# Performance work log

Measured on AMD Instinct MI355X. Metric: run time of the kernel, lower is better.

The kernel has to match this reference:

```python
import jax, jax.numpy as jnp
import numpy as np

HIDDEN = 1280
NUM_HEADS = 16
HEAD_DIM = HIDDEN // NUM_HEADS  # 80
T = 2048
NEG_INF = -1e9


def apply_rope(x, rope):
    # x: [B, T, N, H], rope: [T, H//2]
    half = x.shape[-1] // 2
    xr, xi = x[..., :half], x[..., half:]
    cos = jnp.cos(rope)[None, :, None, :]
    sin = jnp.sin(rope)[None, :, None, :]
    return jnp.concatenate([xr * cos - xi * sin, xr * sin + xi * cos], axis=-1)


def setup_inputs() -> dict:
    key = jax.random.key(0)
    ks = jax.random.split(key, 7)
    x = jax.random.normal(ks[0], (T, 1, HIDDEN), dtype=jnp.float32)
    rotary_pos_emb = jax.random.normal(ks[1], (T, HEAD_DIM // 2), dtype=jnp.float32)
    segment_ids = jnp.sort(jax.random.randint(ks[2], (T,), 0, 8, dtype=jnp.int32))
    s = 0.02
    qkv_kernel = jax.random.normal(ks[3], (HIDDEN, 3 * HIDDEN), dtype=jnp.float32) * s
    qkv_bias = jax.random.normal(ks[4], (3 * HIDDEN,), dtype=jnp.float32) * s
    proj_kernel = jax.random.normal(ks[5], (HIDDEN, HIDDEN), dtype=jnp.float32) * s
    proj_bias = jax.random.normal(ks[6], (HIDDEN,), dtype=jnp.float32) * s
    return {"x": x, "rotary_pos_emb": rotary_pos_emb, "segment_ids": segment_ids,
            "qkv_kernel": qkv_kernel, "qkv_bias": qkv_bias,
            "proj_kernel": proj_kernel, "proj_bias": proj_bias}


def reference(x, rotary_pos_emb, segment_ids, qkv_kernel, qkv_bias, proj_kernel, proj_bias):
    Tt, B, D = x.shape  # B == 1
    N, H = NUM_HEADS, HEAD_DIM
    qkv = x @ qkv_kernel + qkv_bias                      # [T, B, 3D]
    q, k, v = jnp.split(qkv, 3, axis=-1)
    # [T, B, N, H] -> [B, T, N, H]
    q = jnp.transpose(q.reshape(Tt, B, N, H), (1, 0, 2, 3))
    k = jnp.transpose(k.reshape(Tt, B, N, H), (1, 0, 2, 3))
    v = jnp.transpose(v.reshape(Tt, B, N, H), (1, 0, 2, 3))
    q = apply_rope(q, rotary_pos_emb)
    k = apply_rope(k, rotary_pos_emb)
    # segment-masked attention (non-causal), sm_scale = 1/sqrt(H)
    scale = 1.0 / np.sqrt(H).astype(np.float32)
    scores = jnp.einsum('bqnh,bknh->bnqk', q, k) * scale  # [B, N, T, T]
    mask = segment_ids[:, None] == segment_ids[None, :]   # [T, T]
    scores = jnp.where(mask[None, None], scores, NEG_INF)
    probs = jax.nn.softmax(scores, axis=-1)
    out = jnp.einsum('bnqk,bknh->qbnh', probs, v)         # [T, B, N, H]
    out = out.reshape(Tt, B, D)
    return out @ proj_kernel + proj_bias
```

## Files before the change

### kernel.cpp

```cpp
#include <hip/hip_runtime.h>
#include <math.h>

#define TSEQ 2048
#define HIDDEN 1280
#define NH 16
#define HD 80
#define HDP 96
#define ATTN_SCALE 0.11180339887498949f

typedef __bf16 bf16x8 __attribute__((ext_vector_type(8)));
typedef float f32x4 __attribute__((ext_vector_type(4)));

__device__ inline float bf2f(ushort u){ union { unsigned int u; float f; } v; v.u = ((unsigned int)u) << 16; return v.f; }
__device__ inline ushort f2bf(float f){
  union { float f; unsigned int u; } v; v.f = f;
  unsigned int u = v.u;
  return (ushort)((u + 0x7fffu + ((u >> 16) & 1u)) >> 16);
}
__device__ inline float ldin(const void* p, size_t i, bool f32){
  return f32 ? ((const float*)p)[i] : bf2f(((const ushort*)p)[i]);
}
__device__ inline void gl_lds16(const ushort* gp, ushort* lds_base){
  __builtin_amdgcn_global_load_lds(
      (const __attribute__((address_space(1))) unsigned int*)gp,
      (__attribute__((address_space(3))) unsigned int*)lds_base, 16, 0, 0);
}

__global__ void misc_k(const ushort* __restrict__ X, const int* __restrict__ seg,
                       int* __restrict__ flag, int* __restrict__ segS, int* __restrict__ segE){
  int b = blockIdx.x, tid = threadIdx.x;
  if (b == 0){
    int insane = 0;
    for (int i = tid; i < 2048; i += 256){
      ushort u = X[i];
      int e = (u >> 7) & 0xFF;
      int m = u & 0x7F;
      bool bad = (e >= 0xC0) || (e != 0 && e <= 0x30) || (e == 0 && m != 0);
      if (bad) insane++;
    }
    __shared__ int s[256];
    s[tid] = insane; __syncthreads();
    for (int st = 128; st > 0; st >>= 1){ if (tid < st) s[tid] += s[tid + st]; __syncthreads(); }
    if (tid == 0) *flag = (s[0] > 128) ? 1 : 0;
  } else {
    int t = (b - 1) * 256 + tid;
    int id = seg[t];
    int lo = 0, hi = TSEQ;
    while (lo < hi){ int mid = (lo + hi) >> 1; if (seg[mid] < id) lo = mid + 1; else hi = mid; }
    segS[t] = lo;
    lo = 0; hi = TSEQ;
    while (lo < hi){ int mid = (lo + hi) >> 1; if (seg[mid] <= id) lo = mid + 1; else hi = mid; }
    segE[t] = lo;
  }
}

__global__ void prep_k(const int* __restrict__ flag, const void* __restrict__ X,
                       const void* __restrict__ Wq, const void* __restrict__ Wp,
                       ushort* __restrict__ Xb, ushort* __restrict__ WT1, ushort* __restrict__ WT2){
  __shared__ ushort tile[32][33];
  const bool f32 = (*flag != 0);
  int b = blockIdx.x, tid = threadIdx.x;
  if (b < 2560){
    int i = (b * 256 + tid) * 4;
    ushort o[4];
    if (f32){
      float4 v = *reinterpret_cast<const float4*>((const float*)X + i);
      o[0] = f2bf(v.x); o[1] = f2bf(v.y); o[2] = f2bf(v.z); o[3] = f2bf(v.w);
    } else {
      *reinterpret_cast<ushort4*>(o) = *reinterpret_cast<const ushort4*>((const ushort*)X + i);
    }
    *reinterpret_cast<ushort4*>(Xb + i) = *reinterpret_cast<ushort4*>(o);
    return;
  }
  const void* in; ushort* out; int rows, cols, tb;
  if (b < 7360){ tb = b - 2560; in = Wq; out = WT1; rows = HIDDEN; cols = 3 * HIDDEN; }
  else         { tb = b - 7360; in = Wp; out = WT2; rows = HIDDEN; cols = HIDDEN; }
  int tpr = cols / 32;
  int bx = (tb % tpr) * 32, by = (tb / tpr) * 32;
  int tx = tid & 31, ty = tid >> 5;
  for (int i = ty; i < 32; i += 8){
    size_t idx = (size_t)(by + i) * cols + bx + tx;
    tile[i][tx] = f32 ? f2bf(((const float*)in)[idx]) : ((const ushort*)in)[idx];
  }
  __syncthreads();
  for (int i = ty; i < 32; i += 8)
    out[(size_t)(bx + i) * rows + by + tx] = tile[tx][i];
}

template<int MODE>
__launch_bounds__(256, 2)
__global__ void gemm_k(const ushort* __restrict__ A, const ushort* __restrict__ BT,
                       const void* __restrict__ bias, int K, int N,
                       const int* __restrict__ flagp, void* __restrict__ out)
{
  __shared__ __align__(16) ushort As[128 * 64];
  __shared__ __align__(16) ushort Bs[128 * 64];
  const int tid = threadIdx.x;
  const int wave = tid >> 6, lane = tid & 63;
  const int quad = lane >> 4, c = lane & 15;
  const int m0 = blockIdx.y * 128, n0 = blockIdx.x * 128;
  const int wm = (wave & 1) * 64, wn = (wave >> 1) * 64;

  f32x4 acc[4][4];
  for (int i = 0; i < 4; i++) for (int j = 0; j < 4; j++) acc[i][j] = (f32x4){0.f,0.f,0.f,0.f};

  const int drow = lane >> 3;
  const int dcg  = lane & 7;
  const int L8   = ((dcg ^ drow) * 8);
  const ushort* Ab = A  + (size_t)(m0 + wave * 32 + drow) * K + L8;
  const ushort* Bb = BT + (size_t)(n0 + wave * 32 + drow) * K + L8;
  ushort* AsW = As + wave * 32 * 64;
  ushort* BsW = Bs + wave * 32 * 64;
  const size_t row8 = (size_t)8 * K;

  for (int k0 = 0; k0 < K; k0 += 64){
    for (int d = 0; d < 4; d++){
      gl_lds16(Ab + d * row8 + k0, AsW + d * 512);
      gl_lds16(Bb + d * row8 + k0, BsW + d * 512);
    }
    __syncthreads();
    for (int ks = 0; ks < 2; ks++){
      const int pq8 = (((ks * 4 + quad) ^ (c & 7)) * 8);
      bf16x8 af[4], bfv[4];
      for (int i = 0; i < 4; i++) af[i]  = *reinterpret_cast<const bf16x8*>(&As[(wm + i*16 + c) * 64 + pq8]);
      for (int j = 0; j < 4; j++) bfv[j] = *reinterpret_cast<const bf16x8*>(&Bs[(wn + j*16 + c) * 64 + pq8]);
      for (int i = 0; i < 4; i++)
        for (int j = 0; j < 4; j++)
          acc[i][j] = __builtin_amdgcn_mfma_f32_16x16x32_bf16(af[i], bfv[j], acc[i][j], 0, 0, 0);
    }
    __syncthreads();
  }

  const bool f32 = (*flagp != 0);

  for (int j = 0; j < 4; j++){
    int n = n0 + wn + j*16 + c;
    float bv = ldin(bias, n, f32);
    for (int i = 0; i < 4; i++){
      int mbase = m0 + wm + i*16 + quad*4;
      for (int rr = 0; rr < 4; rr++){
        float v = acc[i][j][rr] + bv;
        size_t idx = (size_t)(mbase + rr) * N + n;
        if (MODE == 1 && f32) ((float*)out)[idx] = v;
        else                  ((ushort*)out)[idx] = f2bf(v);
      }
    }
  }
}

__global__ void reshape_k(const int* __restrict__ flag, const ushort* __restrict__ qkv,
                          const void* __restrict__ rope,
                          ushort* __restrict__ Qh, ushort* __restrict__ Kh, ushort* __restrict__ Vt){
  __shared__ __align__(16) ushort shm[5632];
  int b = blockIdx.x, tid = threadIdx.x;
  if (b < 2048){
    ushort* row = shm;
    ushort* rrow = shm + 3840;
    int t = b;
    for (int i = tid; i < 480; i += 256)
      *reinterpret_cast<uint4*>(&row[i * 8]) = *reinterpret_cast<const uint4*>(qkv + (size_t)t * 3840 + i * 8);
    if (tid < 40)
      rrow[tid] = f2bf(ldin(rope, t * 40 + tid, *flag != 0));
    __syncthreads();
    int w = tid;
    if (w < 160){
      int part = w / 80;
      int hw = w - part * 80;
      int h = hw / 5, dr0 = (hw % 5) * 8;
      const ushort* src = &row[part * HIDDEN + h * HD];
      ushort* dst = (part ? Kh : Qh) + ((size_t)h * TSEQ + t) * HDP;
      ushort o0[8], o1[8];
      for (int d = 0; d < 8; d++){
        float th = bf2f(rrow[dr0 + d]);
        float cs = cosf(th), sn = sinf(th);
        float xr = bf2f(src[dr0 + d]);
        float xi = bf2f(src[dr0 + d + 40]);
        o0[d] = f2bf(xr * cs - xi * sn);
        o1[d] = f2bf(xr * sn + xi * cs);
      }
      *reinterpret_cast<uint4*>(dst + dr0)      = *reinterpret_cast<uint4*>(o0);
      *reinterpret_cast<uint4*>(dst + dr0 + 40) = *reinterpret_cast<uint4*>(o1);
    } else if (w < 224){
      int idx = w - 160;
      int part = idx >> 5;
      int h = (idx & 31) >> 1, sg = idx & 1;
      ushort* dst = (part ? Kh : Qh) + ((size_t)h * TSEQ + t) * HDP + 80 + sg * 8;
      uint4 z = {0, 0, 0, 0};
      *reinterpret_cast<uint4*>(dst) = z;
    }
  } else {
    int vb = b - 2048;
    int h = vb & 15, t0 = (vb >> 4) * 64;
    const ushort* src = qkv + 2 * HIDDEN + h * HD;
    for (int w = tid; w < 640; w += 256){
      int r = w / 10, cc = (w % 10) * 8;
      *reinterpret_cast<uint4*>(&shm[r * 88 + cc]) = *reinterpret_cast<const uint4*>(src + (size_t)(t0 + r) * 3840 + cc);
    }
    __syncthreads();
    for (int w = tid; w < 320; w += 256){
      int d = w >> 2, sg = (w & 3) * 16;
      ushort tmp[16];
      for (int i = 0; i < 16; i++) tmp[i] = shm[(sg + i) * 88 + d];
      ushort* dst = Vt + ((size_t)h * HD + d) * TSEQ + t0 + sg;
      *reinterpret_cast<uint4*>(dst)     = *reinterpret_cast<uint4*>(tmp);
      *reinterpret_cast<uint4*>(dst + 8) = *reinterpret_cast<uint4*>(tmp + 8);
    }
  }
}

__launch_bounds__(128, 4)
__global__ void attn_k(const ushort* __restrict__ Qh, const ushort* __restrict__ Kh,
                       const ushort* __restrict__ Vt, const int* __restrict__ seg,
                       const int* __restrict__ segS, const int* __restrict__ segE,
                       ushort* __restrict__ Oh)
{
  __shared__ __align__(16) ushort Pm[2][2][512];
  __shared__ float accS[5][64][4];
  __shared__ float lsumS[64][4];
  int tid = threadIdx.x;
  int wave = tid >> 6, lane = tid & 63;
  int quad = lane >> 4, c = lane & 15;
  int b = blockIdx.x;
  int xcd = b & 7, slot = b >> 3;
  int h = slot & 15;
  int t0 = (xcd * 16 + (slot >> 4)) * 16;

  const ushort* Qb = Qh + (size_t)h * TSEQ * HDP;
  const ushort* Kb = Kh + (size_t)h * TSEQ * HDP;
  const ushort* Vb = Vt + (size_t)h * HD * TSEQ;

  bf16x8 aq[3];
  for (int i = 0; i < 3; i++)
    aq[i] = *reinterpret_cast<const bf16x8*>(Qb + (size_t)(t0 + c) * HDP + i * 32 + quad * 8);

  int segq[4];
  for (int rr = 0; rr < 4; rr++) segq[rr] = seg[t0 + quad * 4 + rr];

  int kstart = segS[t0] & ~31;
  int kend   = segE[t0 + 15];

  float lsum[4] = {0.f, 0.f, 0.f, 0.f};
  f32x4 accd[5];
  for (int dt = 0; dt < 5; dt++) accd[dt] = (f32x4){0.f,0.f,0.f,0.f};

  for (int kt = kstart + wave * 32; kt < kend; kt += 64){
    ushort* pm = &Pm[wave][(kt >> 6) & 1][0];
    f32x4 s0 = (f32x4){0.f,0.f,0.f,0.f}, s1 = (f32x4){0.f,0.f,0.f,0.f};
    for (int i = 0; i < 3; i++){
      bf16x8 bk0 = *reinterpret_cast<const bf16x8*>(Kb + (size_t)(kt + c) * HDP + i * 32 + quad * 8);
      s0 = __builtin_amdgcn_mfma_f32_16x16x32_bf16(aq[i], bk0, s0, 0, 0, 0);
      bf16x8 bk1 = *reinterpret_cast<const bf16x8*>(Kb + (size_t)(kt + 16 + c) * HDP + i * 32 + quad * 8);
      s1 = __builtin_amdgcn_mfma_f32_16x16x32_bf16(aq[i], bk1, s1, 0, 0, 0);
    }
    int segk0 = seg[kt + c];
    int segk1 = seg[kt + 16 + c];
    for (int rr = 0; rr < 4; rr++){
      bool ok0 = (segq[rr] == segk0);
      bool ok1 = (segq[rr] == segk1);
      float e0 = ok0 ? __expf(fminf(s0[rr] * ATTN_SCALE, 30.f)) : 0.f;
      float e1 = ok1 ? __expf(fminf(s1[rr] * ATTN_SCALE, 30.f)) : 0.f;
      ushort u0 = f2bf(e0), u1 = f2bf(e1);
      lsum[rr] += bf2f(u0) + bf2f(u1);
      pm[(quad * 4 + rr) * 32 + c]      = u0;
      pm[(quad * 4 + rr) * 32 + 16 + c] = u1;
    }
    __builtin_amdgcn_s_waitcnt(0xc07f);
    __builtin_amdgcn_wave_barrier();
    bf16x8 pa = *reinterpret_cast<const bf16x8*>(pm + c * 32 + quad * 8);
    for (int dt = 0; dt < 5; dt++){
      bf16x8 bv = *reinterpret_cast<const bf16x8*>(Vb + (size_t)(dt * 16 + c) * TSEQ + kt + quad * 8);
      accd[dt] = __builtin_amdgcn_mfma_f32_16x16x32_bf16(pa, bv, accd[dt], 0, 0, 0);
    }
  }

  if (wave == 1){
    for (int dt = 0; dt < 5; dt++)
      for (int rr = 0; rr < 4; rr++) accS[dt][lane][rr] = accd[dt][rr];
    for (int rr = 0; rr < 4; rr++) lsumS[lane][rr] = lsum[rr];
  }
  __syncthreads();
  if (wave == 0){
    for (int dt = 0; dt < 5; dt++)
      for (int rr = 0; rr < 4; rr++) accd[dt][rr] += accS[dt][lane][rr];
    for (int rr = 0; rr < 4; rr++) lsum[rr] += lsumS[lane][rr];

    float inv[4];
    for (int rr = 0; rr < 4; rr++){
      float rs = lsum[rr];
      rs += __shfl_xor(rs, 1);
      rs += __shfl_xor(rs, 2);
      rs += __shfl_xor(rs, 4);
      rs += __shfl_xor(rs, 8);
      inv[rr] = (rs > 0.f) ? 1.0f / rs : 0.f;
    }
    for (int dt = 0; dt < 5; dt++)
      for (int rr = 0; rr < 4; rr++){
        int t = t0 + quad * 4 + rr;
        Oh[(size_t)t * HIDDEN + h * HD + dt * 16 + c] = f2bf(accd[dt][rr] * inv[rr]);
      }
  }
}

extern "C" void kernel_launch(void* const* d_in, const int* in_sizes, int n_in,
                              void* d_out, int out_size, void* d_ws, size_t ws_size,
                              hipStream_t stream)
{
  const void* X    = d_in[0];
  const void* rope = d_in[1];
  const int*  seg  = (const int*)d_in[2];
  const void* Wq   = d_in[3];
  const void* bq   = d_in[4];
  const void* Wp   = d_in[5];
  const void* bp   = d_in[6];

  char* ws = (char*)d_ws;
  size_t off = 0;
  auto alloc = [&](size_t bytes){ void* p = ws + off; off += (bytes + 255) & ~(size_t)255; return p; };
  int*    flag = (int*)alloc(4);
  int*    segS = (int*)alloc(TSEQ * 4);
  int*    segE = (int*)alloc(TSEQ * 4);
  ushort* Xb   = (ushort*)alloc((size_t)TSEQ * HIDDEN * 2);
  ushort* Qh   = (ushort*)alloc((size_t)NH * TSEQ * HDP * 2);
  ushort* Kh   = (ushort*)alloc((size_t)NH * TSEQ * HDP * 2);
  ushort* Vt   = (ushort*)alloc((size_t)NH * HD * TSEQ * 2);
  ushort* WT1  = (ushort*)alloc((size_t)3 * HIDDEN * HIDDEN * 2);
  ushort* WT2  = (ushort*)alloc((size_t)HIDDEN * HIDDEN * 2);
  ushort* qkv  = (ushort*)alloc((size_t)TSEQ * 3 * HIDDEN * 2);
  ushort* Oh   = Xb;

  misc_k<<<9, 256, 0, stream>>>((const ushort*)X, seg, flag, segS, segE);
  prep_k<<<8960, 256, 0, stream>>>(flag, X, Wq, Wp, Xb, WT1, WT2);
  gemm_k<0><<<dim3(30, 16), 256, 0, stream>>>(Xb, WT1, bq, HIDDEN, 3 * HIDDEN, flag, qkv);
  reshape_k<<<2560, 256, 0, stream>>>(flag, qkv, rope, Qh, Kh, Vt);
  attn_k<<<2048, 128, 0, stream>>>(Qh, Kh, Vt, seg, segS, segE, Oh);
  gemm_k<1><<<dim3(10, 16), 256, 0, stream>>>(Oh, WT2, bp, HIDDEN, HIDDEN, flag, d_out);
}
```

Before: 218.9 us.

## Double-buffer GEMM LDS tiles to overlap global loads with MFMA

The bf16 GEMM kernel now keeps two LDS buffers for A and B and issues the global-to-LDS loads for the next K tile before computing on the current one. Explicit waitcnt/barrier asm replaces __syncthreads so only the older loads are waited on. The aim is to hide global memory latency behind the MFMA work. In exchange, LDS use doubles to 64KB per block, which may limit the 2-blocks-per-CU occupancy, and the hand-written vmcnt counts must match the compiler's load ordering.

```diff
diff --git a/kernel.cpp b/kernel.cpp
--- a/kernel.cpp
+++ b/kernel.cpp
@@ -93,8 +93,8 @@
                        const void* __restrict__ bias, int K, int N,
                        const int* __restrict__ flagp, void* __restrict__ out)
 {
-  __shared__ __align__(16) ushort As[128 * 64];
-  __shared__ __align__(16) ushort Bs[128 * 64];
+  __shared__ __align__(16) ushort As[2][128 * 64];
+  __shared__ __align__(16) ushort Bs[2][128 * 64];
   const int tid = threadIdx.x;
   const int wave = tid >> 6, lane = tid & 63;
   const int quad = lane >> 4, c = lane & 15;
@@ -109,26 +109,39 @@
   const int L8   = ((dcg ^ drow) * 8);
   const ushort* Ab = A  + (size_t)(m0 + wave * 32 + drow) * K + L8;
   const ushort* Bb = BT + (size_t)(n0 + wave * 32 + drow) * K + L8;
-  ushort* AsW = As + wave * 32 * 64;
-  ushort* BsW = Bs + wave * 32 * 64;
   const size_t row8 = (size_t)8 * K;
-
+  const int woff = wave * 32 * 64;
+
+  for (int d = 0; d < 4; d++){
+    gl_lds16(Ab + d * row8, As[0] + woff + d * 512);
+    gl_lds16(Bb + d * row8, Bs[0] + woff + d * 512);
+  }
+
+  int cur = 0;
   for (int k0 = 0; k0 < K; k0 += 64){
-    for (int d = 0; d < 4; d++){
-      gl_lds16(Ab + d * row8 + k0, AsW + d * 512);
-      gl_lds16(Bb + d * row8 + k0, BsW + d * 512);
-    }
-    __syncthreads();
+    if (k0 + 64 < K){
+      int nxt = cur ^ 1;
+      for (int d = 0; d < 4; d++){
+        gl_lds16(Ab + d * row8 + k0 + 64, As[nxt] + woff + d * 512);
+        gl_lds16(Bb + d * row8 + k0 + 64, Bs[nxt] + woff + d * 512);
+      }
+      asm volatile("s_waitcnt vmcnt(8)\ns_barrier" ::: "memory");
+    } else {
+      asm volatile("s_waitcnt vmcnt(0)\ns_barrier" ::: "memory");
+    }
+    const ushort* Ac = As[cur];
+    const ushort* Bc = Bs[cur];
     for (int ks = 0; ks < 2; ks++){
       const int pq8 = (((ks * 4 + quad) ^ (c & 7)) * 8);
       bf16x8 af[4], bfv[4];
-      for (int i = 0; i < 4; i++) af[i]  = *reinterpret_cast<const bf16x8*>(&As[(wm + i*16 + c) * 64 + pq8]);
-      for (int j = 0; j < 4; j++) bfv[j] = *reinterpret_cast<const bf16x8*>(&Bs[(wn + j*16 + c) * 64 + pq8]);
+      for (int i = 0; i < 4; i++) af[i]  = *reinterpret_cast<const bf16x8*>(&Ac[(wm + i*16 + c) * 64 + pq8]);
+      for (int j = 0; j < 4; j++) bfv[j] = *reinterpret_cast<const bf16x8*>(&Bc[(wn + j*16 + c) * 64 + pq8]);
       for (int i = 0; i < 4; i++)
         for (int j = 0; j < 4; j++)
           acc[i][j] = __builtin_amdgcn_mfma_f32_16x16x32_bf16(af[i], bfv[j], acc[i][j], 0, 0, 0);
     }
-    __syncthreads();
+    asm volatile("s_waitcnt lgkmcnt(0)\ns_barrier" ::: "memory");
+    cur ^= 1;
   }
 
   const bool f32 = (*flagp != 0);
```

New measurement: 206.4 us. 1.06x faster.
